# Kernel optimization log

Measured on AMD Instinct MI355X. Metric: run time of the kernel, lower is better.

## Reference

```python
import jax, jax.numpy as jnp
import numpy as np

N_NODES = 100000


def _sage_conv(x, edge_index, W_l, b_l, W_r):
    # PyG SAGEConv (aggr='mean', root_weight=True):
    #   out = lin_l(mean_{j in N(i)} x_j) + lin_r(x_i)
    src, dst = edge_index[0], edge_index[1]
    msg = x[src]                                            # [E, C] gather
    agg = jax.ops.segment_sum(msg, dst, num_segments=N_NODES)  # [N, C]
    deg = jax.ops.segment_sum(jnp.ones((edge_index.shape[1],), x.dtype), dst,
                              num_segments=N_NODES)
    agg = agg / jnp.maximum(deg, 1.0)[:, None]              # mean aggregation
    return agg @ W_l + b_l + x @ W_r


def setup_inputs() -> dict:
    key = jax.random.key(0)
    ks = jax.random.split(key, 10)
    d, h = 128, 128
    s = 1.0 / np.sqrt(d)
    x = jax.random.normal(ks[0], (N_NODES, d), dtype=jnp.float32)
    edge_index = jax.random.randint(ks[1], (2, 640000), 0, N_NODES, dtype=jnp.int64)
    return {
        "x": x,
        "edge_index": edge_index,
        "W1_l": jax.random.uniform(ks[2], (d, h), jnp.float32, -s, s),
        "b1": jnp.zeros((h,), jnp.float32),
        "W1_r": jax.random.uniform(ks[3], (d, h), jnp.float32, -s, s),
        "W2_l": jax.random.uniform(ks[4], (h, h), jnp.float32, -s, s),
        "b2": jnp.zeros((h,), jnp.float32),
        "W2_r": jax.random.uniform(ks[5], (h, h), jnp.float32, -s, s),
        "W_lin": jax.random.uniform(ks[6], (h, 1), jnp.float32, -s, s),
        "b_lin": jnp.zeros((1,), jnp.float32),
    }


def reference(x, edge_index, W1_l, b1, W1_r, W2_l, b2, W2_r, W_lin, b_lin):
    h = jax.nn.relu(_sage_conv(x, edge_index, W1_l, b1, W1_r))
    h = jax.nn.relu(_sage_conv(h, edge_index, W2_l, b2, W2_r))
    return h @ W_lin + b_lin  # [N, 1]
```

## Files before the change

### kernel.cpp

```cpp
#include <hip/hip_runtime.h>
#include <hip/hip_bf16.h>


#define ND 128
#define KTOT 256
#define CAP 32
#define TM 32
#define AGS 136

typedef __bf16 bf16x8 __attribute__((ext_vector_type(8)));
typedef float floatx16 __attribute__((ext_vector_type(16)));

__device__ inline unsigned short f2bf(float f) {
    union { float f; unsigned u; } v; v.f = f;
    unsigned r = v.u + 0x7fffu + ((v.u >> 16) & 1u);
    return (unsigned short)(r >> 16);
}
__device__ inline float bf_lo(unsigned u) { return __uint_as_float(u << 16); }
__device__ inline float bf_hi(unsigned u) { return __uint_as_float(u & 0xffff0000u); }

__device__ inline bf16x8 ldg_bf8(const unsigned short* p, bool ok) {
    int4 v = {0, 0, 0, 0};
    if (ok) v = *(const int4*)p;
    union { int4 i; bf16x8 b; } u; u.i = v;
    return u.b;
}

__global__ void k_prep_all(const float* __restrict__ x, unsigned short* __restrict__ xbf,
                           int nElems,
                           const float* __restrict__ W1l, const float* __restrict__ W1r,
                           unsigned short* __restrict__ Wt1,
                           const float* __restrict__ W2l, const float* __restrict__ W2r,
                           unsigned short* __restrict__ Wt2,
                           const int* __restrict__ esrc_in, const int* __restrict__ edst_in,
                           int* __restrict__ cnt, int* __restrict__ ebuk, int E) {
    const int t = threadIdx.x;
    const int tid = blockIdx.x * 256 + t;

    const int e = blockIdx.x * 128 + t;
    const bool doE = (t < 128) && (e < E);
    int d0 = 0, s0 = 0;
    if (doE) {
        d0 = edst_in[e];
        s0 = esrc_in[e];
    }

    const int i = tid * 8;
    float4 xa, xc;
    const bool doX = (i < nElems);
    if (doX) {
        xa = *(const float4*)(x + i);
        xc = *(const float4*)(x + i + 4);
    }

    int p0 = -1;
    if (doE) p0 = atomicAdd(&cnt[d0], 1);

    if (doX) {
        uint4 r;
        r.x = (unsigned)f2bf(xa.x) | ((unsigned)f2bf(xa.y) << 16);
        r.y = (unsigned)f2bf(xa.z) | ((unsigned)f2bf(xa.w) << 16);
        r.z = (unsigned)f2bf(xc.x) | ((unsigned)f2bf(xc.y) << 16);
        r.w = (unsigned)f2bf(xc.z) | ((unsigned)f2bf(xc.w) << 16);
        *(uint4*)(xbf + i) = r;
    }

    if (tid < 2 * KTOT * ND) {
        const int half = tid >> 15;
        const int idx = tid & 32767;
        const int nn = idx >> 8;
        const int kk = idx & 255;
        const float* Wl = half ? W2l : W1l;
        const float* Wr = half ? W2r : W1r;
        unsigned short* Wt = half ? Wt2 : Wt1;
        float v = (kk < 128) ? Wl[(size_t)kk * ND + nn] : Wr[(size_t)(kk - 128) * ND + nn];
        Wt[(size_t)nn * KTOT + kk] = f2bf(v);
    }

    if (p0 >= 0 && p0 < CAP) ebuk[d0 * CAP + p0] = s0;
}

__device__ __forceinline__ void gatherTM(const unsigned short* __restrict__ feat,
                                         const int* __restrict__ cnt,
                                         const int* __restrict__ ebuk,
                                         int n, int m0, int t,
                                         unsigned short* Agg) {
    const int l = t & 15;
    const int g = t >> 4;
#pragma unroll
    for (int p = 0; p < TM / 16; ++p) {
        const int nl = p * 16 + g;
        const int node = m0 + nl;
        int d = 0;
        if (node < n) d = cnt[node];
        const int dd = min(d, CAP);
        const int* lst = ebuk + (size_t)node * CAP;
        float a0 = 0, a1 = 0, a2 = 0, a3 = 0, a4 = 0, a5 = 0, a6 = 0, a7 = 0;
        const int capi = dd - 1;
        for (int j = 0; j < dd; j += 4) {
            int s0 = lst[j];
            int s1 = lst[min(j + 1, capi)];
            int s2 = lst[min(j + 2, capi)];
            int s3 = lst[min(j + 3, capi)];
            uint4 v0 = ((const uint4*)(feat + (size_t)s0 * ND))[l];
            uint4 v1 = ((const uint4*)(feat + (size_t)s1 * ND))[l];
            uint4 v2 = ((const uint4*)(feat + (size_t)s2 * ND))[l];
            uint4 v3 = ((const uint4*)(feat + (size_t)s3 * ND))[l];
            if (j + 1 >= dd) { v1.x = v1.y = v1.z = v1.w = 0u; }
            if (j + 2 >= dd) { v2.x = v2.y = v2.z = v2.w = 0u; }
            if (j + 3 >= dd) { v3.x = v3.y = v3.z = v3.w = 0u; }
            a0 += bf_lo(v0.x) + bf_lo(v1.x) + bf_lo(v2.x) + bf_lo(v3.x);
            a1 += bf_hi(v0.x) + bf_hi(v1.x) + bf_hi(v2.x) + bf_hi(v3.x);
            a2 += bf_lo(v0.y) + bf_lo(v1.y) + bf_lo(v2.y) + bf_lo(v3.y);
            a3 += bf_hi(v0.y) + bf_hi(v1.y) + bf_hi(v2.y) + bf_hi(v3.y);
            a4 += bf_lo(v0.z) + bf_lo(v1.z) + bf_lo(v2.z) + bf_lo(v3.z);
            a5 += bf_hi(v0.z) + bf_hi(v1.z) + bf_hi(v2.z) + bf_hi(v3.z);
            a6 += bf_lo(v0.w) + bf_lo(v1.w) + bf_lo(v2.w) + bf_lo(v3.w);
            a7 += bf_hi(v0.w) + bf_hi(v1.w) + bf_hi(v2.w) + bf_hi(v3.w);
        }
        float inv = 1.0f / (float)max(d, 1);
        uint4 r;
        r.x = (unsigned)f2bf(a0 * inv) | ((unsigned)f2bf(a1 * inv) << 16);
        r.y = (unsigned)f2bf(a2 * inv) | ((unsigned)f2bf(a3 * inv) << 16);
        r.z = (unsigned)f2bf(a4 * inv) | ((unsigned)f2bf(a5 * inv) << 16);
        r.w = (unsigned)f2bf(a6 * inv) | ((unsigned)f2bf(a7 * inv) << 16);
        *(uint4*)&Agg[nl * AGS + l * 8] = r;
    }
}

__launch_bounds__(256, 4)
__global__ void k_layer1_fused(const unsigned short* __restrict__ feat,
                               const unsigned short* __restrict__ Wt,
                               const float* __restrict__ bias,
                               const int* __restrict__ cnt,
                               const int* __restrict__ ebuk,
                               unsigned short* __restrict__ out, int n) {
    __shared__ __align__(16) unsigned short Agg[TM * AGS];
    const int t = threadIdx.x;
    const int m0 = blockIdx.x * TM;

    gatherTM(feat, cnt, ebuk, n, m0, t, Agg);
    __syncthreads();

    const int wave = t >> 6, lane = t & 63;
    const int l31 = lane & 31, lhalf = lane >> 5;
    const int wn = wave * 32;

    floatx16 acc = (floatx16)0.0f;

#pragma unroll
    for (int kc = 0; kc < 4; ++kc) {
        const int k0 = kc * 32;
        bf16x8 af[2], bfr[2];
#pragma unroll
        for (int ks = 0; ks < 2; ++ks) {
            af[ks]  = *(const bf16x8*)&Agg[l31 * AGS + k0 + ks * 16 + lhalf * 8];
            bfr[ks] = *(const bf16x8*)(Wt + (size_t)(wn + l31) * KTOT + k0 + ks * 16 + lhalf * 8);
        }
        acc = __builtin_amdgcn_mfma_f32_32x32x16_bf16(af[0], bfr[0], acc, 0, 0, 0);
        acc = __builtin_amdgcn_mfma_f32_32x32x16_bf16(af[1], bfr[1], acc, 0, 0, 0);
    }

    const int rA0 = m0 + l31;
    const bool okA = rA0 < n;
#pragma unroll
    for (int kc = 4; kc < 8; ++kc) {
        const int k0 = kc * 32;
        const int ka = k0 - 128;
        bf16x8 af[2], bfr[2];
#pragma unroll
        for (int ks = 0; ks < 2; ++ks) {
            af[ks]  = ldg_bf8(feat + (size_t)rA0 * ND + ka + ks * 16 + lhalf * 8, okA);
            bfr[ks] = *(const bf16x8*)(Wt + (size_t)(wn + l31) * KTOT + k0 + ks * 16 + lhalf * 8);
        }
        acc = __builtin_amdgcn_mfma_f32_32x32x16_bf16(af[0], bfr[0], acc, 0, 0, 0);
        acc = __builtin_amdgcn_mfma_f32_32x32x16_bf16(af[1], bfr[1], acc, 0, 0, 0);
    }

    const int c = wn + l31;
    const float bv = bias[c];
#pragma unroll
    for (int reg = 0; reg < 16; ++reg) {
        const int row = m0 + lhalf * 4 + (reg & 3) + 8 * (reg >> 2);
        if (row < n) {
            float v = fmaxf(acc[reg] + bv, 0.f);
            out[(size_t)row * ND + c] = f2bf(v);
        }
    }
}

__launch_bounds__(256, 4)
__global__ void k_layer2_fused_head(const unsigned short* __restrict__ feat,
                                    const unsigned short* __restrict__ Wt,
                                    const float* __restrict__ bias,
                                    const float* __restrict__ Wlin,
                                    const float* __restrict__ blin,
                                    const int* __restrict__ cnt,
                                    const int* __restrict__ ebuk,
                                    float* __restrict__ out, int n) {
    __shared__ __align__(16) unsigned short Agg[TM * AGS];
    __shared__ float part[TM][4];
    const int t = threadIdx.x;
    const int m0 = blockIdx.x * TM;

    gatherTM(feat, cnt, ebuk, n, m0, t, Agg);
    __syncthreads();

    const int wave = t >> 6, lane = t & 63;
    const int l31 = lane & 31, lhalf = lane >> 5;
    const int wn = wave * 32;

    floatx16 acc = (floatx16)0.0f;

#pragma unroll
    for (int kc = 0; kc < 4; ++kc) {
        const int k0 = kc * 32;
        bf16x8 af[2], bfr[2];
#pragma unroll
        for (int ks = 0; ks < 2; ++ks) {
            af[ks]  = *(const bf16x8*)&Agg[l31 * AGS + k0 + ks * 16 + lhalf * 8];
            bfr[ks] = *(const bf16x8*)(Wt + (size_t)(wn + l31) * KTOT + k0 + ks * 16 + lhalf * 8);
        }
        acc = __builtin_amdgcn_mfma_f32_32x32x16_bf16(af[0], bfr[0], acc, 0, 0, 0);
        acc = __builtin_amdgcn_mfma_f32_32x32x16_bf16(af[1], bfr[1], acc, 0, 0, 0);
    }

    const int rA0 = m0 + l31;
    const bool okA = rA0 < n;
#pragma unroll
    for (int kc = 4; kc < 8; ++kc) {
        const int k0 = kc * 32;
        const int ka = k0 - 128;
        bf16x8 af[2], bfr[2];
#pragma unroll
        for (int ks = 0; ks < 2; ++ks) {
            af[ks]  = ldg_bf8(feat + (size_t)rA0 * ND + ka + ks * 16 + lhalf * 8, okA);
            bfr[ks] = *(const bf16x8*)(Wt + (size_t)(wn + l31) * KTOT + k0 + ks * 16 + lhalf * 8);
        }
        acc = __builtin_amdgcn_mfma_f32_32x32x16_bf16(af[0], bfr[0], acc, 0, 0, 0);
        acc = __builtin_amdgcn_mfma_f32_32x32x16_bf16(af[1], bfr[1], acc, 0, 0, 0);
    }

    const int c = wn + l31;
    const float bv = bias[c];
    const float wv = Wlin[c];
    float p[16];
#pragma unroll
    for (int reg = 0; reg < 16; ++reg)
        p[reg] = fmaxf(acc[reg] + bv, 0.f) * wv;
#pragma unroll
    for (int reg = 0; reg < 16; ++reg) {
        float v = p[reg];
        v += __shfl_xor(v, 1);
        v += __shfl_xor(v, 2);
        v += __shfl_xor(v, 4);
        v += __shfl_xor(v, 8);
        v += __shfl_xor(v, 16);
        if (l31 == 0) {
            int rl = lhalf * 4 + (reg & 3) + 8 * (reg >> 2);
            part[rl][wave] = v;
        }
    }
    __syncthreads();
    if (t < TM) {
        int row = m0 + t;
        if (row < n)
            out[row] = part[t][0] + part[t][1] + part[t][2] + part[t][3] + blin[0];
    }
}

extern "C" void kernel_launch(void* const* d_in, const int* in_sizes, int n_in,
                              void* d_out, int out_size, void* d_ws, size_t ws_size,
                              hipStream_t stream) {
    const float* x    = (const float*)d_in[0];
    const int*   edge = (const int*)d_in[1];
    const float* W1l  = (const float*)d_in[2];
    const float* b1   = (const float*)d_in[3];
    const float* W1r  = (const float*)d_in[4];
    const float* W2l  = (const float*)d_in[5];
    const float* b2   = (const float*)d_in[6];
    const float* W2r  = (const float*)d_in[7];
    const float* Wlin = (const float*)d_in[8];
    const float* blin = (const float*)d_in[9];
    float* out = (float*)d_out;

    int n = out_size;
    int E = in_sizes[1] / 2;
    (void)n_in; (void)ws_size;

    char* ws = (char*)d_ws;
    size_t off = 0;
    auto take = [&](size_t bytes) -> char* {
        char* p = ws + off;
        off += (bytes + 255) & ~(size_t)255;
        return p;
    };
    int* cnt    = (int*)take((size_t)n * 4);
    int* ebuk   = (int*)take((size_t)n * CAP * 4);
    unsigned short* xbf  = (unsigned short*)take((size_t)n * ND * 2);
    unsigned short* h1bf = (unsigned short*)take((size_t)n * ND * 2);
    unsigned short* Wt1  = (unsigned short*)take((size_t)ND * KTOT * 2);
    unsigned short* Wt2  = (unsigned short*)take((size_t)ND * KTOT * 2);

    hipMemsetAsync(cnt, 0, (size_t)n * 4, stream);

    const int* esrc_in = edge;
    const int* edst_in = edge + E;

    int nElems = n * ND;
    int prepBlocks = (nElems / 8 + 255) / 256;

    k_prep_all<<<prepBlocks, 256, 0, stream>>>(
        x, xbf, nElems, W1l, W1r, Wt1, W2l, W2r, Wt2,
        esrc_in, edst_in, cnt, ebuk, E);

    int gemmBlocks = (n + TM - 1) / TM;

    k_layer1_fused<<<gemmBlocks, 256, 0, stream>>>(xbf, Wt1, b1, cnt, ebuk, h1bf, n);
    k_layer2_fused_head<<<gemmBlocks, 256, 0, stream>>>(h1bf, Wt2, b2, Wlin, blin, cnt, ebuk, out, n);
}
```

Before: 250.3 us.

## Pre-swizzle weights into MFMA fragment order and stage self features in LDS

Weight transposition in the prep kernel now writes bf16 weights directly in per-wave MFMA fragment order, so each lane's B-operand load is a contiguous 16-byte read from a coalesced block. Self features for the tile are staged into a second LDS buffer with coalesced row loads, replacing strided per-lane global loads inside the MFMA loop, and the two K halves merge into one loop. Launch bounds rise to 8 blocks per CU to raise occupancy, at the cost of extra LDS per block and a tighter register budget.

```diff
diff --git a/kernel.cpp b/kernel.cpp
--- a/kernel.cpp
+++ b/kernel.cpp
@@ -18,13 +18,6 @@
 }
 __device__ inline float bf_lo(unsigned u) { return __uint_as_float(u << 16); }
 __device__ inline float bf_hi(unsigned u) { return __uint_as_float(u & 0xffff0000u); }
-
-__device__ inline bf16x8 ldg_bf8(const unsigned short* p, bool ok) {
-    int4 v = {0, 0, 0, 0};
-    if (ok) v = *(const int4*)p;
-    union { int4 i; bf16x8 b; } u; u.i = v;
-    return u.b;
-}
 
 __global__ void k_prep_all(const float* __restrict__ x, unsigned short* __restrict__ xbf,
                            int nElems,
@@ -74,7 +67,9 @@
         const float* Wr = half ? W2r : W1r;
         unsigned short* Wt = half ? Wt2 : Wt1;
         float v = (kk < 128) ? Wl[(size_t)kk * ND + nn] : Wr[(size_t)(kk - 128) * ND + nn];
-        Wt[(size_t)nn * KTOT + kk] = f2bf(v);
+        const int n32 = nn >> 5, r = nn & 31;
+        const int kc = kk >> 5, ks = (kk >> 4) & 1, lh = (kk >> 3) & 1, k8 = kk & 7;
+        Wt[n32 * 8192 + kc * 1024 + ks * 512 + (lh * 32 + r) * 8 + k8] = f2bf(v);
     }
 
     if (p0 >= 0 && p0 < CAP) ebuk[d0 * CAP + p0] = s0;
@@ -128,7 +123,22 @@
     }
 }
 
-__launch_bounds__(256, 4)
+__device__ __forceinline__ void stageSelf(const unsigned short* __restrict__ feat,
+                                          int n, int m0, int t,
+                                          unsigned short* Sf) {
+#pragma unroll
+    for (int q = 0; q < (TM * ND / 8) / 256; ++q) {
+        const int idx = t + q * 256;
+        const int row = idx >> 4;
+        const int c16 = idx & 15;
+        int4 w = {0, 0, 0, 0};
+        const int gr = m0 + row;
+        if (gr < n) w = *(const int4*)(feat + (size_t)gr * ND + c16 * 8);
+        *(int4*)&Sf[row * AGS + c16 * 8] = w;
+    }
+}
+
+__launch_bounds__(256, 8)
 __global__ void k_layer1_fused(const unsigned short* __restrict__ feat,
                                const unsigned short* __restrict__ Wt,
                                const float* __restrict__ bias,
@@ -136,42 +146,31 @@
                                const int* __restrict__ ebuk,
                                unsigned short* __restrict__ out, int n) {
     __shared__ __align__(16) unsigned short Agg[TM * AGS];
+    __shared__ __align__(16) unsigned short Sf[TM * AGS];
     const int t = threadIdx.x;
     const int m0 = blockIdx.x * TM;
 
     gatherTM(feat, cnt, ebuk, n, m0, t, Agg);
+    stageSelf(feat, n, m0, t, Sf);
     __syncthreads();
 
     const int wave = t >> 6, lane = t & 63;
     const int l31 = lane & 31, lhalf = lane >> 5;
     const int wn = wave * 32;
+    const unsigned short* Bw = Wt + wave * 8192;
 
     floatx16 acc = (floatx16)0.0f;
 
 #pragma unroll
-    for (int kc = 0; kc < 4; ++kc) {
-        const int k0 = kc * 32;
+    for (int kc = 0; kc < 8; ++kc) {
+        const unsigned short* Ab = (kc < 4)
+            ? &Agg[l31 * AGS + kc * 32]
+            : &Sf[l31 * AGS + (kc - 4) * 32];
         bf16x8 af[2], bfr[2];
 #pragma unroll
         for (int ks = 0; ks < 2; ++ks) {
-            af[ks]  = *(const bf16x8*)&Agg[l31 * AGS + k0 + ks * 16 + lhalf * 8];
-            bfr[ks] = *(const bf16x8*)(Wt + (size_t)(wn + l31) * KTOT + k0 + ks * 16 + lhalf * 8);
-        }
-        acc = __builtin_amdgcn_mfma_f32_32x32x16_bf16(af[0], bfr[0], acc, 0, 0, 0);
-        acc = __builtin_amdgcn_mfma_f32_32x32x16_bf16(af[1], bfr[1], acc, 0, 0, 0);
-    }
-
-    const int rA0 = m0 + l31;
-    const bool okA = rA0 < n;
-#pragma unroll
-    for (int kc = 4; kc < 8; ++kc) {
-        const int k0 = kc * 32;
-        const int ka = k0 - 128;
-        bf16x8 af[2], bfr[2];
-#pragma unroll
-        for (int ks = 0; ks < 2; ++ks) {
-            af[ks]  = ldg_bf8(feat + (size_t)rA0 * ND + ka + ks * 16 + lhalf * 8, okA);
-            bfr[ks] = *(const bf16x8*)(Wt + (size_t)(wn + l31) * KTOT + k0 + ks * 16 + lhalf * 8);
+            af[ks]  = *(const bf16x8*)(Ab + ks * 16 + lhalf * 8);
+            bfr[ks] = *(const bf16x8*)(Bw + kc * 1024 + ks * 512 + lane * 8);
         }
         acc = __builtin_amdgcn_mfma_f32_32x32x16_bf16(af[0], bfr[0], acc, 0, 0, 0);
         acc = __builtin_amdgcn_mfma_f32_32x32x16_bf16(af[1], bfr[1], acc, 0, 0, 0);
@@ -189,7 +188,7 @@
     }
 }
 
-__launch_bounds__(256, 4)
+__launch_bounds__(256, 8)
 __global__ void k_layer2_fused_head(const unsigned short* __restrict__ feat,
                                     const unsigned short* __restrict__ Wt,
                                     const float* __restrict__ bias,
@@ -199,43 +198,32 @@
                                     const int* __restrict__ ebuk,
                                     float* __restrict__ out, int n) {
     __shared__ __align__(16) unsigned short Agg[TM * AGS];
+    __shared__ __align__(16) unsigned short Sf[TM * AGS];
     __shared__ float part[TM][4];
     const int t = threadIdx.x;
     const int m0 = blockIdx.x * TM;
 
     gatherTM(feat, cnt, ebuk, n, m0, t, Agg);
+    stageSelf(feat, n, m0, t, Sf);
     __syncthreads();
 
     const int wave = t >> 6, lane = t & 63;
     const int l31 = lane & 31, lhalf = lane >> 5;
     const int wn = wave * 32;
+    const unsigned short* Bw = Wt + wave * 8192;
 
     floatx16 acc = (floatx16)0.0f;
 
 #pragma unroll
-    for (int kc = 0; kc < 4; ++kc) {
-        const int k0 = kc * 32;
+    for (int kc = 0; kc < 8; ++kc) {
+        const unsigned short* Ab = (kc < 4)
+            ? &Agg[l31 * AGS + kc * 32]
+            : &Sf[l31 * AGS + (kc - 4) * 32];
         bf16x8 af[2], bfr[2];
 #pragma unroll
         for (int ks = 0; ks < 2; ++ks) {
-            af[ks]  = *(const bf16x8*)&Agg[l31 * AGS + k0 + ks * 16 + lhalf * 8];
-            bfr[ks] = *(const bf16x8*)(Wt + (size_t)(wn + l31) * KTOT + k0 + ks * 16 + lhalf * 8);
-        }
-        acc = __builtin_amdgcn_mfma_f32_32x32x16_bf16(af[0], bfr[0], acc, 0, 0, 0);
-        acc = __builtin_amdgcn_mfma_f32_32x32x16_bf16(af[1], bfr[1], acc, 0, 0, 0);
-    }
-
-    const int rA0 = m0 + l31;
-    const bool okA = rA0 < n;
-#pragma unroll
-    for (int kc = 4; kc < 8; ++kc) {
-        const int k0 = kc * 32;
-        const int ka = k0 - 128;
-        bf16x8 af[2], bfr[2];
-#pragma unroll
-        for (int ks = 0; ks < 2; ++ks) {
-            af[ks]  = ldg_bf8(feat + (size_t)rA0 * ND + ka + ks * 16 + lhalf * 8, okA);
-            bfr[ks] = *(const bf16x8*)(Wt + (size_t)(wn + l31) * KTOT + k0 + ks * 16 + lhalf * 8);
+            af[ks]  = *(const bf16x8*)(Ab + ks * 16 + lhalf * 8);
+            bfr[ks] = *(const bf16x8*)(Bw + kc * 1024 + ks * 512 + lane * 8);
         }
         acc = __builtin_amdgcn_mfma_f32_32x32x16_bf16(af[0], bfr[0], acc, 0, 0, 0);
         acc = __builtin_amdgcn_mfma_f32_32x32x16_bf16(af[1], bfr[1], acc, 0, 0, 0);
```

After: 215.4 us. -14.0%, faster.
